# Kernel tuning notes

Hardware: AMD Instinct MI355X
Metric: run time of the kernel (lower is better)

The kernel has to match this reference:

```python
import jax, jax.numpy as jnp
import numpy as np

# ---- static config (matches init_kwargs) ----
N0, N1 = 150000, 75000          # al nodes, test nodes
E = 200000                       # edges per edge type
D = 128                          # dim_h
L = 3                            # n_layers
T = 4                            # netypes
NAL = 50000                      # n_al vocab
NC = 3                           # n_classes
T_SRCS = [0, 0, 1, 1]
T_TGTS = [0, 1, 0, 1]
NODE_COUNTS = [N0, N1]


def setup_inputs() -> dict:
    key = jax.random.key(0)
    ks = jax.random.split(key, 16)
    x0_ids = jax.random.randint(ks[0], (N0,), 0, NAL, dtype=jnp.int32)
    x1_ids = jnp.zeros((N1,), dtype=jnp.int32)  # emb_test has a single row

    def make_edges(k, n_src, n_dst):
        k1, k2 = jax.random.split(k)
        src = jax.random.randint(k1, (E,), 0, n_src, dtype=jnp.int32)
        dst = jax.random.randint(k2, (E,), 0, n_dst, dtype=jnp.int32)
        return jnp.stack([src, dst])  # [2, E]

    es = [make_edges(ks[1 + j], NODE_COUNTS[T_SRCS[j]], NODE_COUNTS[T_TGTS[j]])
          for j in range(T)]

    s = 1.0 / np.sqrt(D)
    enc_al_w   = jax.random.normal(ks[5],  (NAL, D), jnp.float32) * s
    emb_test_w = jax.random.normal(ks[6],  (1, D),   jnp.float32) * s
    W_tgt = jax.random.normal(ks[7],  (L, T, D, D), jnp.float32) * s
    b_tgt = jax.random.normal(ks[8],  (L, T, D),    jnp.float32) * 0.01
    W_src = jax.random.normal(ks[9],  (L, T, D, D), jnp.float32) * s
    b_src = jax.random.normal(ks[10], (L, T, D),    jnp.float32) * 0.01
    emb_self = jax.random.normal(ks[11], (L, T, 2, D), jnp.float32) * s
    W_dec = jax.random.normal(ks[12], (NC, D), jnp.float32) * s
    b_dec = jax.random.normal(ks[13], (NC,),   jnp.float32) * 0.01
    return {
        "x0_ids": x0_ids, "x1_ids": x1_ids,
        "es0": es[0], "es1": es[1], "es2": es[2], "es3": es[3],
        "enc_al_w": enc_al_w, "emb_test_w": emb_test_w,
        "W_tgt": W_tgt, "b_tgt": b_tgt, "W_src": W_src, "b_src": b_src,
        "emb_self": emb_self, "W_dec": W_dec, "b_dec": b_dec,
    }


def reference(x0_ids, x1_ids, es0, es1, es2, es3,
              enc_al_w, emb_test_w, W_tgt, b_tgt, W_src, b_src,
              emb_self, W_dec, b_dec):
    ess = [es0, es1, es2, es3]
    # node-type embeddings
    xs = [enc_al_w[x0_ids], emb_test_w[x1_ids]]  # [N0,D], [N1,D]
    for i in range(L):
        out = [jnp.zeros((N0, D), xs[0].dtype), jnp.zeros((N1, D), xs[1].dtype)]
        for j in range(T):
            ts, tt = T_SRCS[j], T_TGTS[j]
            src, dst = ess[j][0], ess[j][1]
            # project node features first (same math as projecting gathered edges)
            h_src = xs[ts] @ W_src[i, j].T + b_src[i, j]   # lin_src(x_src)
            h_dst = xs[tt] @ W_tgt[i, j].T + b_tgt[i, j]   # lin_tgt(x_dst)
            self_flag = (dst == src).astype(jnp.int32)
            msg = h_dst[dst] + h_src[src] + emb_self[i, j][self_flag]  # [E,D]
            agg = jax.ops.segment_max(msg, dst, num_segments=NODE_COUNTS[tt])
            out[tt] = out[tt] + jax.nn.relu(agg)  # MPNN.forward applies relu
        xs = [jax.nn.relu(out[0]), jax.nn.relu(out[1])]
    last = xs[0] @ W_dec.T + b_dec                 # [N0, NC]
    return (last, jax.nn.softmax(last, axis=1))
```

## Files before the change

### kernel.cpp

```cpp
#include <hip/hip_runtime.h>
#include <hip/hip_bf16.h>

#define N0 150000
#define N1 75000
#define EE 200000
#define NAL 50000
#define NSEG (N0 + N1)
#define NSEG2 (2 * NSEG)
#define TOTE (4 * EE)

typedef unsigned short u16;
using s16x8 = __attribute__((ext_vector_type(8))) short;
using f32x4 = __attribute__((ext_vector_type(4))) float;
using u16x8 = __attribute__((ext_vector_type(8))) unsigned short;

__device__ __forceinline__ u16 f2b(float f) {
  unsigned int b = __float_as_uint(f);
  b += 0x7FFFu + ((b >> 16) & 1u);
  return (u16)(b >> 16);
}
__device__ __forceinline__ float b2f(u16 u) {
  return __uint_as_float(((unsigned int)u) << 16);
}

__global__ void sentinel_k(float* out, float val) {
  if (threadIdx.x == 0 && blockIdx.x == 0) out[0] = val;
}

__global__ __launch_bounds__(256) void prep_w(const float* __restrict__ Ws,
                                              const float* __restrict__ Wt,
                                              u16* __restrict__ BP) {
  int idx = blockIdx.x * 256 + threadIdx.x;
  int mk = idx & 16383;
  int slot = (idx >> 14) & 7;
  int i = idx >> 17;
  const int ssel[8] = {1, 0, 0, 1, 1, 1, 0, 0};
  const int sj[8]   = {0, 0, 2, 1, 2, 3, 1, 3};
  const float* W = ssel[slot] ? Ws : Wt;
  BP[idx] = f2b(W[(size_t)(i * 4 + sj[slot]) * 16384 + mk]);
}

__global__ __launch_bounds__(256) void embed_k(const int* __restrict__ ids,
                                               const float* __restrict__ tab,
                                               u16* __restrict__ X, int N, unsigned vocab) {
  int idx = blockIdx.x * 256 + threadIdx.x;
  int v = idx >> 4;
  if (v >= N) return;
  int q = (idx & 15) << 3;
  unsigned id = (unsigned)ids[v];
  if (id >= vocab) id = 0;
  const float* src = tab + (size_t)id * 128 + q;
  f32x4 x0 = *(const f32x4*)src;
  f32x4 x1 = *(const f32x4*)(src + 4);
  u16x8 o;
#pragma unroll
  for (int k = 0; k < 4; ++k) { o[k] = f2b(x0[k]); o[4 + k] = f2b(x1[k]); }
  *(u16x8*)(X + (size_t)v * 128 + q) = o;
}

__global__ __launch_bounds__(256) void count_all(const int* __restrict__ e0,
                                                 const int* __restrict__ e1,
                                                 const int* __restrict__ e2,
                                                 const int* __restrict__ e3,
                                                 int* __restrict__ cnt) {
  int i = blockIdx.x * 256 + threadIdx.x;
  if (i >= TOTE) return;
  int j = i / EE, r = i - j * EE;
  const int* es = (j == 0) ? e0 : (j == 1) ? e1 : (j == 2) ? e2 : e3;
  int dst = es[EE + r];
  int seg = (j & 1) ? N0 + dst : dst;
  atomicAdd(cnt + seg * 2 + (j >> 1), 1);
}

__global__ __launch_bounds__(512) void scan1_k(const int* __restrict__ cnt,
                                               int* __restrict__ off,
                                               int* __restrict__ part, int N) {
  __shared__ int sh[512];
  int t = threadIdx.x, i = blockIdx.x * 512 + t;
  int v = (i < N) ? cnt[i] : 0;
  sh[t] = v; __syncthreads();
  for (int s = 1; s < 512; s <<= 1) {
    int x = (t >= s) ? sh[t - s] : 0; __syncthreads();
    sh[t] += x; __syncthreads();
  }
  if (i < N) off[i] = sh[t] - v;
  if (t == 511) part[blockIdx.x] = sh[511];
}

__global__ __launch_bounds__(1024) void scan2_k(int* __restrict__ part, int n) {
  __shared__ int sh[1024];
  int t = threadIdx.x;
  int v = (t < n) ? part[t] : 0;
  sh[t] = v; __syncthreads();
  for (int s = 1; s < 1024; s <<= 1) {
    int x = (t >= s) ? sh[t - s] : 0; __syncthreads();
    sh[t] += x; __syncthreads();
  }
  if (t < n) part[t] = sh[t] - v;
}

__global__ __launch_bounds__(256) void scan3_k(int* __restrict__ off,
                                               const int* __restrict__ part, int N, int tot) {
  int i = blockIdx.x * 256 + threadIdx.x;
  if (i < N) off[i] += part[i >> 9];
  if (i == 0) off[N] = tot;
}

__global__ __launch_bounds__(256) void fill_all(const int* __restrict__ e0,
                                                const int* __restrict__ e1,
                                                const int* __restrict__ e2,
                                                const int* __restrict__ e3,
                                                const int* __restrict__ off,
                                                int* __restrict__ cur,
                                                int* __restrict__ einfo) {
  int i = blockIdx.x * 256 + threadIdx.x;
  if (i >= TOTE) return;
  int j = i / EE, r = i - j * EE;
  const int* es = (j == 0) ? e0 : (j == 1) ? e1 : (j == 2) ? e2 : e3;
  int src = es[r], dst = es[EE + r];
  int seg2 = ((j & 1) ? N0 + dst : dst) * 2 + (j >> 1);
  int pos = off[seg2] + atomicAdd(cur + seg2, 1);
  einfo[pos] = src | ((src == dst) ? (int)0x80000000 : 0);
}

__global__ __launch_bounds__(256, 3) void gemm_multi(const u16* __restrict__ A, int M,
                                                     const u16* __restrict__ W, int nw,
                                                     u16* __restrict__ C0,
                                                     u16* __restrict__ C1,
                                                     u16* __restrict__ C2,
                                                     u16* __restrict__ C3) {
  __shared__ u16 Al[64 * 128];
  __shared__ u16 Bl[128 * 128];
  const int t = threadIdx.x;
  const int row0 = blockIdx.x * 64;

#pragma unroll
  for (int u = 0; u < 4; ++u) {
    int c = u * 256 + t;
    int r = c >> 4, ch = c & 15;
    int sw = ch ^ (r & 7);
    if (row0 + r < M)
      *(u16x8*)&Al[r * 128 + sw * 8] = *(const u16x8*)(A + (size_t)(row0 + r) * 128 + ch * 8);
  }

  const int w = t >> 6, lane = t & 63;
  const int lr = lane & 15, g = lane >> 4;
  const int arow = (w * 16 + lr) * 128;

  for (int ws = 0; ws < nw; ++ws) {
    if (ws) __syncthreads();
    const u16* Bsub = W + (size_t)ws * 16384;
#pragma unroll
    for (int u = 0; u < 8; ++u) {
      int c = u * 256 + t;
      int r = c >> 4, ch = c & 15;
      int sw = ch ^ (r & 7);
      *(u16x8*)&Bl[r * 128 + sw * 8] = *(const u16x8*)(Bsub + r * 128 + ch * 8);
    }
    __syncthreads();

    f32x4 acc[8];
#pragma unroll
    for (int nf = 0; nf < 8; ++nf) acc[nf] = f32x4{0.f, 0.f, 0.f, 0.f};

#pragma unroll
    for (int ks = 0; ks < 4; ++ks) {
      int swz = ((ks * 4 + g) ^ (lr & 7)) * 8;
      s16x8 a = *(const s16x8*)&Al[arow + swz];
#pragma unroll
      for (int nf = 0; nf < 8; ++nf) {
        s16x8 b = *(const s16x8*)&Bl[(nf * 16 + lr) * 128 + swz];
        acc[nf] = __builtin_amdgcn_mfma_f32_16x16x32_bf16(a, b, acc[nf], 0, 0, 0);
      }
    }

    u16* Cw = (ws == 0) ? C0 : (ws == 1) ? C1 : (ws == 2) ? C2 : C3;
#pragma unroll
    for (int nf = 0; nf < 8; ++nf) {
      int col = nf * 16 + lr;
#pragma unroll
      for (int j = 0; j < 4; ++j) {
        int row = row0 + w * 16 + g * 4 + j;
        if (row < M) Cw[(size_t)row * 128 + col] = f2b(acc[nf][j]);
      }
    }
  }
}

__global__ __launch_bounds__(256) void agg2_k(const int* __restrict__ off2,
                                              const int* __restrict__ einfo,
                                              int segbase,
                                              const u16* __restrict__ HSA,
                                              const u16* __restrict__ HSB,
                                              const u16* __restrict__ HD0,
                                              const u16* __restrict__ HD1,
                                              const float* __restrict__ bs0,
                                              const float* __restrict__ bt0,
                                              const float* __restrict__ bs1,
                                              const float* __restrict__ bt1,
                                              const float* __restrict__ esf0,
                                              const float* __restrict__ esf1,
                                              u16* __restrict__ Y, int N) {
  int idx = blockIdx.x * 256 + threadIdx.x;
  int d = idx >> 4;
  if (d >= N) return;
  int f8 = (idx & 15) << 3;
  int base = (segbase + d) * 2;
  int e0 = off2[base], e1 = off2[base + 1], e2 = off2[base + 2];

  float en[8], es_[8];
#pragma unroll
  for (int k = 0; k < 8; ++k) { en[k] = esf0[f8 + k]; es_[k] = esf0[128 + f8 + k]; }
  float m0[8];
#pragma unroll
  for (int k = 0; k < 8; ++k) m0[k] = -INFINITY;
  for (int e = e0; e < e1; ++e) {
    int info = einfo[e];
    int s = info & 0x7fffffff;
    bool self = (info < 0);
    u16x8 hv = *(const u16x8*)(HSA + (size_t)s * 128 + f8);
#pragma unroll
    for (int k = 0; k < 8; ++k)
      m0[k] = fmaxf(m0[k], b2f(hv[k]) + (self ? es_[k] : en[k]));
  }

#pragma unroll
  for (int k = 0; k < 8; ++k) { en[k] = esf1[f8 + k]; es_[k] = esf1[128 + f8 + k]; }
  float m1[8];
#pragma unroll
  for (int k = 0; k < 8; ++k) m1[k] = -INFINITY;
  for (int e = e1; e < e2; ++e) {
    int info = einfo[e];
    int s = info & 0x7fffffff;
    bool self = (info < 0);
    u16x8 hv = *(const u16x8*)(HSB + (size_t)s * 128 + f8);
#pragma unroll
    for (int k = 0; k < 8; ++k)
      m1[k] = fmaxf(m1[k], b2f(hv[k]) + (self ? es_[k] : en[k]));
  }

  u16x8 hd0 = *(const u16x8*)(HD0 + (size_t)d * 128 + f8);
  u16x8 hd1 = *(const u16x8*)(HD1 + (size_t)d * 128 + f8);
  u16x8 o;
#pragma unroll
  for (int k = 0; k < 8; ++k) {
    float r0 = fmaxf(b2f(hd0[k]) + bs0[f8 + k] + bt0[f8 + k] + m0[k], 0.f);
    float r1 = fmaxf(b2f(hd1[k]) + bs1[f8 + k] + bt1[f8 + k] + m1[k], 0.f);
    o[k] = f2b(r0 + r1);
  }
  *(u16x8*)(Y + (size_t)d * 128 + f8) = o;
}

__global__ __launch_bounds__(256) void decoder_k(const u16* __restrict__ X,
                                                 const float* __restrict__ Wd,
                                                 const float* __restrict__ bd,
                                                 float* __restrict__ out) {
  int v = blockIdx.x * 256 + threadIdx.x;
  if (v >= N0) return;
  float a0 = bd[0], a1 = bd[1], a2 = bd[2];
  const u16* x = X + (size_t)v * 128;
#pragma unroll
  for (int k = 0; k < 128; k += 8) {
    u16x8 xv = *(const u16x8*)(x + k);
#pragma unroll
    for (int u = 0; u < 8; ++u) {
      float xf = b2f(xv[u]);
      a0 = fmaf(xf, Wd[k + u], a0);
      a1 = fmaf(xf, Wd[128 + k + u], a1);
      a2 = fmaf(xf, Wd[256 + k + u], a2);
    }
  }
  float mx = fmaxf(a0, fmaxf(a1, a2));
  float e0 = expf(a0 - mx), e1 = expf(a1 - mx), e2 = expf(a2 - mx);
  float inv = 1.f / (e0 + e1 + e2);
  size_t b = (size_t)v * 3;
  out[b + 0] = a0; out[b + 1] = a1; out[b + 2] = a2;
  size_t b2 = (size_t)N0 * 3 + b;
  out[b2 + 0] = e0 * inv; out[b2 + 1] = e1 * inv; out[b2 + 2] = e2 * inv;
}

extern "C" void kernel_launch(void* const* d_in, const int* in_sizes, int n_in,
                              void* d_out, int out_size, void* d_ws, size_t ws_size,
                              hipStream_t stream) {
  float* out = (float*)d_out;

  const int expect[15] = {N0, N1, 2 * EE, 2 * EE, 2 * EE, 2 * EE,
                          NAL * 128, 128, 196608, 1536, 196608, 1536,
                          3072, 384, 3};
  bool ok = (n_in == 15);
  if (ok) for (int i = 0; i < 15; ++i) ok = ok && (in_sizes[i] == expect[i]);
  if (!ok) { sentinel_k<<<1, 64, 0, stream>>>(out, 500.f); return; }

  const int* x0_ids = (const int*)d_in[0];
  const int* x1_ids = (const int*)d_in[1];
  const int* es0 = (const int*)d_in[2];
  const int* es1 = (const int*)d_in[3];
  const int* es2 = (const int*)d_in[4];
  const int* es3 = (const int*)d_in[5];
  const float* enc_al   = (const float*)d_in[6];
  const float* emb_test = (const float*)d_in[7];
  const float* W_tgt    = (const float*)d_in[8];
  const float* b_tgt    = (const float*)d_in[9];
  const float* W_src    = (const float*)d_in[10];
  const float* b_src    = (const float*)d_in[11];
  const float* emb_self = (const float*)d_in[12];
  const float* W_dec    = (const float*)d_in[13];
  const float* b_dec    = (const float*)d_in[14];

  char* base = (char*)d_ws;
  size_t pos = 0;
  auto alloc = [&](size_t bytes) -> void* {
    void* r = base + pos;
    pos += (bytes + 255) & ~(size_t)255;
    return r;
  };
  u16* xs0 = (u16*)alloc((size_t)N0 * 128 * 2);
  u16* xs1 = (u16*)alloc((size_t)N1 * 128 * 2);
  u16* P0  = (u16*)alloc((size_t)N0 * 128 * 2);
  u16* P1  = (u16*)alloc((size_t)N0 * 128 * 2);
  u16* P2  = (u16*)alloc((size_t)N0 * 128 * 2);
  u16* P3  = (u16*)alloc((size_t)N1 * 128 * 2);
  u16* P4  = (u16*)alloc((size_t)N0 * 128 * 2);
  u16* BP  = (u16*)alloc((size_t)3 * 8 * 16384 * 2);
  int* off2   = (int*)alloc((size_t)(NSEG2 + 1) * 4);
  int* einfo  = (int*)alloc((size_t)TOTE * 4);
  int* counts = (int*)alloc((size_t)NSEG2 * 4);
  int* cursor = counts;
  int* part   = (int*)alloc(1024 * 4);
  if (pos > ws_size) { sentinel_k<<<1, 64, 0, stream>>>(out, 900.f); return; }

  prep_w<<<1536, 256, 0, stream>>>(W_src, W_tgt, BP);
  embed_k<<<(N0 * 16 + 255) / 256, 256, 0, stream>>>(x0_ids, enc_al, xs0, N0, NAL);
  embed_k<<<(N1 * 16 + 255) / 256, 256, 0, stream>>>(x1_ids, emb_test, xs1, N1, 1);

  const int EG = (TOTE + 255) / 256;
  const int nb = (NSEG2 + 511) / 512;
  hipMemsetAsync(counts, 0, (size_t)NSEG2 * 4, stream);
  count_all<<<EG, 256, 0, stream>>>(es0, es1, es2, es3, counts);
  scan1_k<<<nb, 512, 0, stream>>>(counts, off2, part, NSEG2);
  scan2_k<<<1, 1024, 0, stream>>>(part, nb);
  scan3_k<<<(NSEG2 + 255) / 256, 256, 0, stream>>>(off2, part, NSEG2, TOTE);
  hipMemsetAsync(cursor, 0, (size_t)NSEG2 * 4, stream);
  fill_all<<<EG, 256, 0, stream>>>(es0, es1, es2, es3, off2, cursor, einfo);

  const int G0 = (N0 + 63) / 64, G1 = (N1 + 63) / 64;
  const int GA0 = (N0 * 16 + 255) / 256, GA1 = (N1 * 16 + 255) / 256;
  for (int i = 0; i < 3; ++i) {
    const u16* BPi = BP + (size_t)i * 8 * 16384;
    gemm_multi<<<G0, 256, 0, stream>>>(xs0, N0, BPi + 0 * 16384, (i < 2) ? 4 : 3,
                                       P0, P1, P2, P4);
    gemm_multi<<<G1, 256, 0, stream>>>(xs1, N1, BPi + 4 * 16384, 1, P3, P3, P3, P3);
    agg2_k<<<GA0, 256, 0, stream>>>(off2, einfo, 0, P0, P3, P1, P2,
                                    b_src + (size_t)(i * 4 + 0) * 128, b_tgt + (size_t)(i * 4 + 0) * 128,
                                    b_src + (size_t)(i * 4 + 2) * 128, b_tgt + (size_t)(i * 4 + 2) * 128,
                                    emb_self + (size_t)(i * 4 + 0) * 256,
                                    emb_self + (size_t)(i * 4 + 2) * 256, xs0, N0);
    if (i < 2) {
      gemm_multi<<<G1, 256, 0, stream>>>(xs1, N1, BPi + 5 * 16384, 3, P3, P1, P2, P2);
      agg2_k<<<GA1, 256, 0, stream>>>(off2, einfo, N0, P4, P3, P1, P2,
                                      b_src + (size_t)(i * 4 + 1) * 128, b_tgt + (size_t)(i * 4 + 1) * 128,
                                      b_src + (size_t)(i * 4 + 3) * 128, b_tgt + (size_t)(i * 4 + 3) * 128,
                                      emb_self + (size_t)(i * 4 + 1) * 256,
                                      emb_self + (size_t)(i * 4 + 3) * 256, xs1, N1);
    }
  }

  decoder_k<<<(N0 + 255) / 256, 256, 0, stream>>>(xs0, W_dec, b_dec, out);
}
```

Baseline: 534.5 us.

## Partition self-loop edges and use order-preserving bf16 integer max in aggregation

The CSR fill now places self-loop edges first in each segment, with a separate self-count array, so the aggregation no longer branches per edge on a self flag. Source projections are stored in a sign-flipped bf16 encoding that makes signed 16-bit integer max order-preserving. The non-self max then runs as a packed s16x8 integer max, with the bias added once after the loop instead of per edge and per element. This costs extra atomics and memsets during CSR construction and one more kernel argument; a segment with no non-self edges comes out as a finite bf16 sentinel rather than -inf.

```diff
diff --git a/kernel.cpp b/kernel.cpp
--- a/kernel.cpp
+++ b/kernel.cpp
@@ -21,6 +21,9 @@
 }
 __device__ __forceinline__ float b2f(u16 u) {
   return __uint_as_float(((unsigned int)u) << 16);
+}
+__device__ __forceinline__ u16 flip16(u16 v) {
+  return v ^ (u16)((((int)(short)v) >> 15) & 0x7FFF);
 }
 
 __global__ void sentinel_k(float* out, float val) {
@@ -62,14 +65,16 @@
                                                  const int* __restrict__ e1,
                                                  const int* __restrict__ e2,
                                                  const int* __restrict__ e3,
-                                                 int* __restrict__ cnt) {
+                                                 int* __restrict__ cnt,
+                                                 int* __restrict__ scnt) {
   int i = blockIdx.x * 256 + threadIdx.x;
   if (i >= TOTE) return;
   int j = i / EE, r = i - j * EE;
   const int* es = (j == 0) ? e0 : (j == 1) ? e1 : (j == 2) ? e2 : e3;
-  int dst = es[EE + r];
-  int seg = (j & 1) ? N0 + dst : dst;
-  atomicAdd(cnt + seg * 2 + (j >> 1), 1);
+  int src = es[r], dst = es[EE + r];
+  int seg2 = ((j & 1) ? N0 + dst : dst) * 2 + (j >> 1);
+  atomicAdd(cnt + seg2, 1);
+  if (src == dst) atomicAdd(scnt + seg2, 1);
 }
 
 __global__ __launch_bounds__(512) void scan1_k(const int* __restrict__ cnt,
@@ -111,7 +116,9 @@
                                                 const int* __restrict__ e2,
                                                 const int* __restrict__ e3,
                                                 const int* __restrict__ off,
+                                                const int* __restrict__ scnt,
                                                 int* __restrict__ cur,
+                                                int* __restrict__ scur,
                                                 int* __restrict__ einfo) {
   int i = blockIdx.x * 256 + threadIdx.x;
   if (i >= TOTE) return;
@@ -119,12 +126,15 @@
   const int* es = (j == 0) ? e0 : (j == 1) ? e1 : (j == 2) ? e2 : e3;
   int src = es[r], dst = es[EE + r];
   int seg2 = ((j & 1) ? N0 + dst : dst) * 2 + (j >> 1);
-  int pos = off[seg2] + atomicAdd(cur + seg2, 1);
-  einfo[pos] = src | ((src == dst) ? (int)0x80000000 : 0);
+  int pos;
+  if (src == dst) pos = off[seg2] + atomicAdd(scur + seg2, 1);
+  else            pos = off[seg2] + scnt[seg2] + atomicAdd(cur + seg2, 1);
+  einfo[pos] = src;
 }
 
 __global__ __launch_bounds__(256, 3) void gemm_multi(const u16* __restrict__ A, int M,
                                                      const u16* __restrict__ W, int nw,
+                                                     int flipmask,
                                                      u16* __restrict__ C0,
                                                      u16* __restrict__ C1,
                                                      u16* __restrict__ C2,
@@ -175,13 +185,18 @@
     }
 
     u16* Cw = (ws == 0) ? C0 : (ws == 1) ? C1 : (ws == 2) ? C2 : C3;
+    const bool flip = (flipmask >> ws) & 1;
 #pragma unroll
     for (int nf = 0; nf < 8; ++nf) {
       int col = nf * 16 + lr;
 #pragma unroll
       for (int j = 0; j < 4; ++j) {
         int row = row0 + w * 16 + g * 4 + j;
-        if (row < M) Cw[(size_t)row * 128 + col] = f2b(acc[nf][j]);
+        if (row < M) {
+          u16 v = f2b(acc[nf][j]);
+          if (flip) v = flip16(v);
+          Cw[(size_t)row * 128 + col] = v;
+        }
       }
     }
   }
@@ -189,6 +204,7 @@
 
 __global__ __launch_bounds__(256) void agg2_k(const int* __restrict__ off2,
                                               const int* __restrict__ einfo,
+                                              const int* __restrict__ scnt,
                                               int segbase,
                                               const u16* __restrict__ HSA,
                                               const u16* __restrict__ HSB,
@@ -206,37 +222,45 @@
   if (d >= N) return;
   int f8 = (idx & 15) << 3;
   int base = (segbase + d) * 2;
-  int e0 = off2[base], e1 = off2[base + 1], e2 = off2[base + 2];
-
-  float en[8], es_[8];
-#pragma unroll
-  for (int k = 0; k < 8; ++k) { en[k] = esf0[f8 + k]; es_[k] = esf0[128 + f8 + k]; }
+  int a = off2[base], b1 = off2[base + 1], c2 = off2[base + 2];
+  int sc0 = scnt[base], sc1 = scnt[base + 1];
+
+  const short NEGINF = (short)0x807F;
+
+  s16x8 mv0 = {NEGINF, NEGINF, NEGINF, NEGINF, NEGINF, NEGINF, NEGINF, NEGINF};
+  for (int e = a + sc0; e < b1; ++e) {
+    int s = einfo[e];
+    s16x8 hv = *(const s16x8*)(HSA + (size_t)s * 128 + f8);
+    mv0 = __builtin_elementwise_max(mv0, hv);
+  }
   float m0[8];
 #pragma unroll
-  for (int k = 0; k < 8; ++k) m0[k] = -INFINITY;
-  for (int e = e0; e < e1; ++e) {
-    int info = einfo[e];
-    int s = info & 0x7fffffff;
-    bool self = (info < 0);
+  for (int k = 0; k < 8; ++k)
+    m0[k] = b2f(flip16((u16)mv0[k])) + esf0[f8 + k];
+  for (int e = a; e < a + sc0; ++e) {
+    int s = einfo[e];
     u16x8 hv = *(const u16x8*)(HSA + (size_t)s * 128 + f8);
 #pragma unroll
     for (int k = 0; k < 8; ++k)
-      m0[k] = fmaxf(m0[k], b2f(hv[k]) + (self ? es_[k] : en[k]));
-  }
-
-#pragma unroll
-  for (int k = 0; k < 8; ++k) { en[k] = esf1[f8 + k]; es_[k] = esf1[128 + f8 + k]; }
+      m0[k] = fmaxf(m0[k], b2f(flip16(hv[k])) + esf0[128 + f8 + k]);
+  }
+
+  s16x8 mv1 = {NEGINF, NEGINF, NEGINF, NEGINF, NEGINF, NEGINF, NEGINF, NEGINF};
+  for (int e = b1 + sc1; e < c2; ++e) {
+    int s = einfo[e];
+    s16x8 hv = *(const s16x8*)(HSB + (size_t)s * 128 + f8);
+    mv1 = __builtin_elementwise_max(mv1, hv);
+  }
   float m1[8];
 #pragma unroll
-  for (int k = 0; k < 8; ++k) m1[k] = -INFINITY;
-  for (int e = e1; e < e2; ++e) {
-    int info = einfo[e];
-    int s = info & 0x7fffffff;
-    bool self = (info < 0);
+  for (int k = 0; k < 8; ++k)
+    m1[k] = b2f(flip16((u16)mv1[k])) + esf1[f8 + k];
+  for (int e = b1; e < b1 + sc1; ++e) {
+    int s = einfo[e];
     u16x8 hv = *(const u16x8*)(HSB + (size_t)s * 128 + f8);
 #pragma unroll
     for (int k = 0; k < 8; ++k)
-      m1[k] = fmaxf(m1[k], b2f(hv[k]) + (self ? es_[k] : en[k]));
+      m1[k] = fmaxf(m1[k], b2f(flip16(hv[k])) + esf1[128 + f8 + k]);
   }
 
   u16x8 hd0 = *(const u16x8*)(HD0 + (size_t)d * 128 + f8);
@@ -325,6 +349,8 @@
   int* off2   = (int*)alloc((size_t)(NSEG2 + 1) * 4);
   int* einfo  = (int*)alloc((size_t)TOTE * 4);
   int* counts = (int*)alloc((size_t)NSEG2 * 4);
+  int* scnt   = (int*)alloc((size_t)NSEG2 * 4);
+  int* scur   = (int*)alloc((size_t)NSEG2 * 4);
   int* cursor = counts;
   int* part   = (int*)alloc(1024 * 4);
   if (pos > ws_size) { sentinel_k<<<1, 64, 0, stream>>>(out, 900.f); return; }
@@ -336,28 +362,30 @@
   const int EG = (TOTE + 255) / 256;
   const int nb = (NSEG2 + 511) / 512;
   hipMemsetAsync(counts, 0, (size_t)NSEG2 * 4, stream);
-  count_all<<<EG, 256, 0, stream>>>(es0, es1, es2, es3, counts);
+  hipMemsetAsync(scnt, 0, (size_t)NSEG2 * 4, stream);
+  count_all<<<EG, 256, 0, stream>>>(es0, es1, es2, es3, counts, scnt);
   scan1_k<<<nb, 512, 0, stream>>>(counts, off2, part, NSEG2);
   scan2_k<<<1, 1024, 0, stream>>>(part, nb);
   scan3_k<<<(NSEG2 + 255) / 256, 256, 0, stream>>>(off2, part, NSEG2, TOTE);
   hipMemsetAsync(cursor, 0, (size_t)NSEG2 * 4, stream);
-  fill_all<<<EG, 256, 0, stream>>>(es0, es1, es2, es3, off2, cursor, einfo);
+  hipMemsetAsync(scur, 0, (size_t)NSEG2 * 4, stream);
+  fill_all<<<EG, 256, 0, stream>>>(es0, es1, es2, es3, off2, scnt, cursor, scur, einfo);
 
   const int G0 = (N0 + 63) / 64, G1 = (N1 + 63) / 64;
   const int GA0 = (N0 * 16 + 255) / 256, GA1 = (N1 * 16 + 255) / 256;
   for (int i = 0; i < 3; ++i) {
     const u16* BPi = BP + (size_t)i * 8 * 16384;
     gemm_multi<<<G0, 256, 0, stream>>>(xs0, N0, BPi + 0 * 16384, (i < 2) ? 4 : 3,
-                                       P0, P1, P2, P4);
-    gemm_multi<<<G1, 256, 0, stream>>>(xs1, N1, BPi + 4 * 16384, 1, P3, P3, P3, P3);
-    agg2_k<<<GA0, 256, 0, stream>>>(off2, einfo, 0, P0, P3, P1, P2,
+                                       0b1001, P0, P1, P2, P4);
+    gemm_multi<<<G1, 256, 0, stream>>>(xs1, N1, BPi + 4 * 16384, 1, 1, P3, P3, P3, P3);
+    agg2_k<<<GA0, 256, 0, stream>>>(off2, einfo, scnt, 0, P0, P3, P1, P2,
                                     b_src + (size_t)(i * 4 + 0) * 128, b_tgt + (size_t)(i * 4 + 0) * 128,
                                     b_src + (size_t)(i * 4 + 2) * 128, b_tgt + (size_t)(i * 4 + 2) * 128,
                                     emb_self + (size_t)(i * 4 + 0) * 256,
                                     emb_self + (size_t)(i * 4 + 2) * 256, xs0, N0);
     if (i < 2) {
-      gemm_multi<<<G1, 256, 0, stream>>>(xs1, N1, BPi + 5 * 16384, 3, P3, P1, P2, P2);
-      agg2_k<<<GA1, 256, 0, stream>>>(off2, einfo, N0, P4, P3, P1, P2,
+      gemm_multi<<<G1, 256, 0, stream>>>(xs1, N1, BPi + 5 * 16384, 3, 1, P3, P1, P2, P2);
+      agg2_k<<<GA1, 256, 0, stream>>>(off2, einfo, scnt, N0, P4, P3, P1, P2,
                                       b_src + (size_t)(i * 4 + 1) * 128, b_tgt + (size_t)(i * 4 + 1) * 128,
                                       b_src + (size_t)(i * 4 + 3) * 128, b_tgt + (size_t)(i * 4 + 3) * 128,
                                       emb_self + (size_t)(i * 4 + 1) * 256,
```

New measurement: 548.3 us. 2.6% more time.
